# Kernel tuning notes

Measured on AMD Instinct MI355X. Metric: run time of the kernel, lower is better.

Reference implementation:

```python
import jax, jax.numpy as jnp
import numpy as np
from jax import lax

M, B, D = 32, 64, 8192  # history length, batch of systems, degrees of freedom


def setup_inputs() -> dict:
    key = jax.random.key(0)
    k1, k2, k3 = jax.random.split(key, 3)
    s = jax.random.normal(k1, (M, B, D), dtype=jnp.float32)
    y = jax.random.normal(k2, (M, B, D), dtype=jnp.float32)
    frc = jax.random.normal(k3, (B, D), dtype=jnp.float32)
    return {"s": s, "y": y, "frc": frc}


def reference(s, y, frc):
    # r_i = 1 / (s_i . y_i), per batch row, as stored by extend()
    r = 1.0 / jnp.sum(s * y, axis=-1, keepdims=True)  # [M, B, 1]

    # First loop: iterate history from newest (i = M-1) to oldest (i = 0)
    def back_step(q, carry):
        si, yi, ri = carry
        ai = ri * jnp.sum(si * q, axis=-1, keepdims=True)  # [B, 1]
        q = q - ai * yi
        return q, ai

    q0 = -frc
    q, a_rev = lax.scan(back_step, q0, (s[::-1], y[::-1], r[::-1]))
    a = a_rev[::-1]  # a[i] now aligned with history index i

    # Initial Hessian scaling gamma = (s_last . y_last) / (y_last . y_last)
    g = (jnp.sum(s[-1] * y[-1], axis=-1) / jnp.sum(y[-1] * y[-1], axis=-1))[:, None]
    q = g * q

    # Second loop: oldest to newest
    def fwd_step(q, carry):
        si, yi, ri, ai = carry
        bi = ri * jnp.sum(yi * q, axis=-1, keepdims=True)
        q = q + si * (ai - bi)
        return q, None

    q, _ = lax.scan(fwd_step, q, (s, y, r, a))
    return -q
```

## Files before the change

### kernel.cpp

```cpp
#include <hip/hip_runtime.h>

#define Mh 32
#define Bh 64
#define Dh 8192
#define KCH 1024
#define NCH (Dh / KCH)

#define OFF_WSY 0
#define OFF_WYY (64 * 1024)
#define OFF_VS  (2 * 64 * 1024)
#define OFF_VY  (OFF_VS + 64 * 32)
#define OFF_CY  (OFF_VY + 64 * 32)
#define OFF_CS  (OFF_CY + 64 * 32)
#define OFF_G   (OFF_CS + 64 * 32)
#define WS_ZERO_FLOATS OFF_CY

__global__ __launch_bounds__(256) void gram_kernel(
    const float* __restrict__ s, const float* __restrict__ y,
    const float* __restrict__ frc, float* __restrict__ ws)
{
    __shared__ float sT[32 * 64];
    __shared__ float yT[32 * 64];
    __shared__ float fT[64];

    const int b  = blockIdx.x & 63;
    const int ch = blockIdx.x >> 6;
    const int k0 = ch * KCH;
    const int t  = threadIdx.x;
    const int w  = t >> 6;
    const int l  = t & 63;
    const int tx = l & 7;
    const int ty = l >> 3;

    float asy[4][4] = {};
    float ayy[4][4] = {};
    float avs[4] = {}, avy[4] = {};

    const int i0 = t >> 4,          k4_0 = t & 15;
    const int i1 = (t + 256) >> 4,  k4_1 = (t + 256) & 15;

    for (int st = 0; st < KCH / 64; ++st) {
        const int kb = k0 + st * 64;
        const float4 sv0 = *(const float4*)(s + ((size_t)i0 * Bh + b) * Dh + kb + (k4_0 << 2));
        const float4 yv0 = *(const float4*)(y + ((size_t)i0 * Bh + b) * Dh + kb + (k4_0 << 2));
        const float4 sv1 = *(const float4*)(s + ((size_t)i1 * Bh + b) * Dh + kb + (k4_1 << 2));
        const float4 yv1 = *(const float4*)(y + ((size_t)i1 * Bh + b) * Dh + kb + (k4_1 << 2));
        float4 fv4 = make_float4(0.f, 0.f, 0.f, 0.f);
        if (t < 16) fv4 = *(const float4*)(frc + (size_t)b * Dh + kb + (t << 2));

        __syncthreads();
        {
            const int kk0 = (k4_0 << 2) ^ (((i0 >> 2) & 7) << 2);
            *(float4*)&sT[i0 * 64 + kk0] = sv0;
            *(float4*)&yT[i0 * 64 + kk0] = yv0;
            const int kk1 = (k4_1 << 2) ^ (((i1 >> 2) & 7) << 2);
            *(float4*)&sT[i1 * 64 + kk1] = sv1;
            *(float4*)&yT[i1 * 64 + kk1] = yv1;
            if (t < 16) *(float4*)&fT[t << 2] = fv4;
        }
        __syncthreads();

        #pragma unroll
        for (int kk = 0; kk < 16; kk += 4) {
            const int kc = (w << 4) + kk;
            float4 sv[4], ytv[4], yxv[4];
            #pragma unroll
            for (int aa = 0; aa < 4; ++aa) {
                sv[aa]  = *(const float4*)&sT[((ty << 2) + aa) * 64 + (kc ^ (ty << 2))];
                ytv[aa] = *(const float4*)&yT[((ty << 2) + aa) * 64 + (kc ^ (ty << 2))];
                yxv[aa] = *(const float4*)&yT[((tx << 2) + aa) * 64 + (kc ^ (tx << 2))];
            }
            const float4 fv = *(const float4*)&fT[kc];
            #pragma unroll
            for (int aa = 0; aa < 4; ++aa) {
                #pragma unroll
                for (int cc = 0; cc < 4; ++cc) {
                    asy[aa][cc] += sv[aa].x * yxv[cc].x + sv[aa].y * yxv[cc].y
                                 + sv[aa].z * yxv[cc].z + sv[aa].w * yxv[cc].w;
                    ayy[aa][cc] += ytv[aa].x * yxv[cc].x + ytv[aa].y * yxv[cc].y
                                 + ytv[aa].z * yxv[cc].z + ytv[aa].w * yxv[cc].w;
                }
                avs[aa] += sv[aa].x * fv.x + sv[aa].y * fv.y + sv[aa].z * fv.z + sv[aa].w * fv.w;
                avy[aa] += ytv[aa].x * fv.x + ytv[aa].y * fv.y + ytv[aa].z * fv.z + ytv[aa].w * fv.w;
            }
        }
    }

    __syncthreads();
    for (int wv = 0; wv < 4; ++wv) {
        if (w == wv) {
            #pragma unroll
            for (int aa = 0; aa < 4; ++aa) {
                #pragma unroll
                for (int cc = 0; cc < 4; ++cc) {
                    const int e = ((ty << 2) + aa) * 32 + (tx << 2) + cc;
                    if (wv == 0) { sT[e] = asy[aa][cc];  yT[e] = ayy[aa][cc]; }
                    else         { sT[e] += asy[aa][cc]; yT[e] += ayy[aa][cc]; }
                }
                if (tx == 0) {
                    const int i = (ty << 2) + aa;
                    if (wv == 0) { fT[i] = avs[aa];  fT[32 + i] = avy[aa]; }
                    else         { fT[i] += avs[aa]; fT[32 + i] += avy[aa]; }
                }
            }
        }
        __syncthreads();
    }

    float* WSY = ws + OFF_WSY + b * 1024;
    float* WYY = ws + OFF_WYY + b * 1024;
    for (int e = t; e < 1024; e += 256) {
        unsafeAtomicAdd(&WSY[e], sT[e]);
        unsafeAtomicAdd(&WYY[e], yT[e]);
    }
    if (t < 32)      unsafeAtomicAdd(&ws[OFF_VS + b * 32 + t], fT[t]);
    else if (t < 64) unsafeAtomicAdd(&ws[OFF_VY + b * 32 + (t - 32)], fT[t]);
}

__global__ __launch_bounds__(64) void recur_kernel(float* __restrict__ ws)
{
    const int b    = blockIdx.x;
    const int lane = threadIdx.x;
    const int i    = lane & 31;

    const float* WSY = ws + OFF_WSY + b * 1024;
    const float* WYY = ws + OFF_WYY + b * 1024;

    float row_sy[32], col_sy[32], row_yy[32];
    #pragma unroll
    for (int j = 0; j < 32; ++j) {
        row_sy[j] = WSY[i * 32 + j];
        col_sy[j] = WSY[j * 32 + i];
        row_yy[j] = WYY[i * 32 + j];
    }

    const double r = 1.0 / (double)row_sy[i];
    double acc = -(double)ws[OFF_VS + b * 32 + i];
    double a_val = 0.0;
    #pragma unroll
    for (int j = 31; j >= 0; --j) {
        const double aj = __shfl(r, j) * __shfl(acc, j);
        if (i == j) a_val = aj;
        if (i < j)  acc -= aj * (double)row_sy[j];
    }

    const double g = (double)WSY[31 * 32 + 31] / (double)WYY[31 * 32 + 31];

    double u = -(double)ws[OFF_VY + b * 32 + i];
    #pragma unroll
    for (int j = 0; j < 32; ++j)
        u -= __shfl(a_val, j) * (double)row_yy[j];
    u *= g;

    double tt = u;
    double b_val = 0.0;
    #pragma unroll
    for (int j = 0; j < 32; ++j) {
        const double bj = __shfl(r, j) * __shfl(tt, j);
        if (i == j) b_val = bj;
        const double dj = __shfl(a_val, j) - bj;
        if (i > j) tt += dj * (double)col_sy[j];
    }

    if (lane < 32) {
        ws[OFF_CY + b * 32 + i] = (float)(g * a_val);
        ws[OFF_CS + b * 32 + i] = (float)(b_val - a_val);
    }
    if (lane == 0) ws[OFF_G + b] = (float)g;
}

__global__ __launch_bounds__(256) void combine_kernel(
    const float* __restrict__ s, const float* __restrict__ y,
    const float* __restrict__ frc, const float* __restrict__ ws,
    float* __restrict__ out)
{
    __shared__ float cy[32], cs[32];
    const int b  = blockIdx.x & 63;
    const int ch = blockIdx.x >> 6;
    const int t  = threadIdx.x;
    if (t < 32) { cy[t] = ws[OFF_CY + b * 32 + t]; cs[t] = ws[OFF_CS + b * 32 + t]; }
    __syncthreads();

    const int d = ch * 1024 + (t << 2);
    const float g = ws[OFF_G + b];
    const float4 fv = *(const float4*)(frc + (size_t)b * Dh + d);
    float4 acc;
    acc.x = g * fv.x; acc.y = g * fv.y; acc.z = g * fv.z; acc.w = g * fv.w;

    #pragma unroll 8
    for (int i = 0; i < 32; ++i) {
        const float4 yv = *(const float4*)(y + ((size_t)i * Bh + b) * Dh + d);
        const float4 sv = *(const float4*)(s + ((size_t)i * Bh + b) * Dh + d);
        const float a1 = cy[i], a2 = cs[i];
        acc.x += a1 * yv.x + a2 * sv.x;
        acc.y += a1 * yv.y + a2 * sv.y;
        acc.z += a1 * yv.z + a2 * sv.z;
        acc.w += a1 * yv.w + a2 * sv.w;
    }
    *(float4*)(out + (size_t)b * Dh + d) = acc;
}

extern "C" void kernel_launch(void* const* d_in, const int* in_sizes, int n_in,
                              void* d_out, int out_size, void* d_ws, size_t ws_size,
                              hipStream_t stream)
{
    const float* s   = (const float*)d_in[0];
    const float* y   = (const float*)d_in[1];
    const float* frc = (const float*)d_in[2];
    float* out = (float*)d_out;
    float* ws  = (float*)d_ws;

    hipMemsetAsync(d_ws, 0, (size_t)WS_ZERO_FLOATS * sizeof(float), stream);

    gram_kernel<<<dim3(Bh * NCH), dim3(256), 0, stream>>>(s, y, frc, ws);
    recur_kernel<<<dim3(Bh), dim3(64), 0, stream>>>(ws);
    combine_kernel<<<dim3(Bh * NCH), dim3(256), 0, stream>>>(s, y, frc, ws, out);
}
```

Measured before the change: 232.7 us.

## Prefetch gram tiles, replace atomics with partial buffers, batch combine loads

The gram kernel now stages 128-wide tiles and issues the global loads for the next stage into registers while computing the current one. Per-chunk partial Gram matrices are written to separate workspace slots instead of being atomically accumulated. This removes the memset and the atomics, and the recurrence kernel now reduces the eight partials in shared memory. The combine kernel groups 8 history loads at a time to raise memory-level parallelism. The trade-offs are more registers, more LDS, and an extra workspace read in the recurrence kernel.

```diff
diff --git a/kernel.cpp b/kernel.cpp
--- a/kernel.cpp
+++ b/kernel.cpp
@@ -5,23 +5,24 @@
 #define Dh 8192
 #define KCH 1024
 #define NCH (Dh / KCH)
-
-#define OFF_WSY 0
-#define OFF_WYY (64 * 1024)
-#define OFF_VS  (2 * 64 * 1024)
-#define OFF_VY  (OFF_VS + 64 * 32)
-#define OFF_CY  (OFF_VY + 64 * 32)
-#define OFF_CS  (OFF_CY + 64 * 32)
-#define OFF_G   (OFF_CS + 64 * 32)
-#define WS_ZERO_FLOATS OFF_CY
+#define STG 128
+#define NST (KCH / STG)
+
+#define OFF_PSY 0
+#define OFF_PYY 524288
+#define OFF_PVS 1048576
+#define OFF_PVY (OFF_PVS + 16384)
+#define OFF_CY  (OFF_PVY + 16384)
+#define OFF_CS  (OFF_CY + 2048)
+#define OFF_G   (OFF_CS + 2048)
 
 __global__ __launch_bounds__(256) void gram_kernel(
     const float* __restrict__ s, const float* __restrict__ y,
     const float* __restrict__ frc, float* __restrict__ ws)
 {
-    __shared__ float sT[32 * 64];
-    __shared__ float yT[32 * 64];
-    __shared__ float fT[64];
+    __shared__ float sT[32 * STG];
+    __shared__ float yT[32 * STG];
+    __shared__ float fT[STG];
 
     const int b  = blockIdx.x & 63;
     const int ch = blockIdx.x >> 6;
@@ -31,57 +32,66 @@
     const int l  = t & 63;
     const int tx = l & 7;
     const int ty = l >> 3;
+    const size_t base = (size_t)b * Dh;
 
     float asy[4][4] = {};
     float ayy[4][4] = {};
     float avs[4] = {}, avy[4] = {};
 
-    const int i0 = t >> 4,          k4_0 = t & 15;
-    const int i1 = (t + 256) >> 4,  k4_1 = (t + 256) & 15;
-
-    for (int st = 0; st < KCH / 64; ++st) {
-        const int kb = k0 + st * 64;
-        const float4 sv0 = *(const float4*)(s + ((size_t)i0 * Bh + b) * Dh + kb + (k4_0 << 2));
-        const float4 yv0 = *(const float4*)(y + ((size_t)i0 * Bh + b) * Dh + kb + (k4_0 << 2));
-        const float4 sv1 = *(const float4*)(s + ((size_t)i1 * Bh + b) * Dh + kb + (k4_1 << 2));
-        const float4 yv1 = *(const float4*)(y + ((size_t)i1 * Bh + b) * Dh + kb + (k4_1 << 2));
-        float4 fv4 = make_float4(0.f, 0.f, 0.f, 0.f);
-        if (t < 16) fv4 = *(const float4*)(frc + (size_t)b * Dh + kb + (t << 2));
-
+    int ri[4], rc[4];
+    #pragma unroll
+    for (int rep = 0; rep < 4; ++rep) {
+        const int idx = t + rep * 256;
+        ri[rep] = idx >> 5;
+        rc[rep] = idx & 31;
+    }
+
+    float4 pS[4], pY[4], pF;
+    auto issue = [&](int kb) {
+        #pragma unroll
+        for (int rep = 0; rep < 4; ++rep) {
+            const size_t off = ((size_t)ri[rep] * Bh) * Dh + base + kb + (rc[rep] << 2);
+            pS[rep] = *(const float4*)(s + off);
+            pY[rep] = *(const float4*)(y + off);
+        }
+        if (t < 32) pF = *(const float4*)(frc + base + kb + (t << 2));
+    };
+
+    issue(k0);
+    for (int st = 0; st < NST; ++st) {
         __syncthreads();
-        {
-            const int kk0 = (k4_0 << 2) ^ (((i0 >> 2) & 7) << 2);
-            *(float4*)&sT[i0 * 64 + kk0] = sv0;
-            *(float4*)&yT[i0 * 64 + kk0] = yv0;
-            const int kk1 = (k4_1 << 2) ^ (((i1 >> 2) & 7) << 2);
-            *(float4*)&sT[i1 * 64 + kk1] = sv1;
-            *(float4*)&yT[i1 * 64 + kk1] = yv1;
-            if (t < 16) *(float4*)&fT[t << 2] = fv4;
-        }
+        #pragma unroll
+        for (int rep = 0; rep < 4; ++rep) {
+            const int col = rc[rep] ^ ((ri[rep] >> 2) & 7);
+            *(float4*)&sT[ri[rep] * STG + (col << 2)] = pS[rep];
+            *(float4*)&yT[ri[rep] * STG + (col << 2)] = pY[rep];
+        }
+        if (t < 32) *(float4*)&fT[t << 2] = pF;
         __syncthreads();
-
-        #pragma unroll
-        for (int kk = 0; kk < 16; kk += 4) {
-            const int kc = (w << 4) + kk;
-            float4 sv[4], ytv[4], yxv[4];
+        if (st + 1 < NST) issue(k0 + (st + 1) * STG);
+
+        #pragma unroll
+        for (int kk = 0; kk < 8; ++kk) {
+            const int c0 = (w << 3) + kk;
+            float4 sv[4], tv[4], xv[4];
             #pragma unroll
             for (int aa = 0; aa < 4; ++aa) {
-                sv[aa]  = *(const float4*)&sT[((ty << 2) + aa) * 64 + (kc ^ (ty << 2))];
-                ytv[aa] = *(const float4*)&yT[((ty << 2) + aa) * 64 + (kc ^ (ty << 2))];
-                yxv[aa] = *(const float4*)&yT[((tx << 2) + aa) * 64 + (kc ^ (tx << 2))];
+                sv[aa] = *(const float4*)&sT[((ty << 2) + aa) * STG + ((c0 ^ ty) << 2)];
+                tv[aa] = *(const float4*)&yT[((ty << 2) + aa) * STG + ((c0 ^ ty) << 2)];
+                xv[aa] = *(const float4*)&yT[((tx << 2) + aa) * STG + ((c0 ^ tx) << 2)];
             }
-            const float4 fv = *(const float4*)&fT[kc];
+            const float4 fv = *(const float4*)&fT[c0 << 2];
             #pragma unroll
             for (int aa = 0; aa < 4; ++aa) {
                 #pragma unroll
                 for (int cc = 0; cc < 4; ++cc) {
-                    asy[aa][cc] += sv[aa].x * yxv[cc].x + sv[aa].y * yxv[cc].y
-                                 + sv[aa].z * yxv[cc].z + sv[aa].w * yxv[cc].w;
-                    ayy[aa][cc] += ytv[aa].x * yxv[cc].x + ytv[aa].y * yxv[cc].y
-                                 + ytv[aa].z * yxv[cc].z + ytv[aa].w * yxv[cc].w;
+                    asy[aa][cc] += sv[aa].x * xv[cc].x + sv[aa].y * xv[cc].y
+                                 + sv[aa].z * xv[cc].z + sv[aa].w * xv[cc].w;
+                    ayy[aa][cc] += tv[aa].x * xv[cc].x + tv[aa].y * xv[cc].y
+                                 + tv[aa].z * xv[cc].z + tv[aa].w * xv[cc].w;
                 }
                 avs[aa] += sv[aa].x * fv.x + sv[aa].y * fv.y + sv[aa].z * fv.z + sv[aa].w * fv.w;
-                avy[aa] += ytv[aa].x * fv.x + ytv[aa].y * fv.y + ytv[aa].z * fv.z + ytv[aa].w * fv.w;
+                avy[aa] += tv[aa].x * fv.x + tv[aa].y * fv.y + tv[aa].z * fv.z + tv[aa].w * fv.w;
             }
         }
     }
@@ -107,25 +117,44 @@
         __syncthreads();
     }
 
-    float* WSY = ws + OFF_WSY + b * 1024;
-    float* WYY = ws + OFF_WYY + b * 1024;
-    for (int e = t; e < 1024; e += 256) {
-        unsafeAtomicAdd(&WSY[e], sT[e]);
-        unsafeAtomicAdd(&WYY[e], yT[e]);
-    }
-    if (t < 32)      unsafeAtomicAdd(&ws[OFF_VS + b * 32 + t], fT[t]);
-    else if (t < 64) unsafeAtomicAdd(&ws[OFF_VY + b * 32 + (t - 32)], fT[t]);
-}
-
-__global__ __launch_bounds__(64) void recur_kernel(float* __restrict__ ws)
-{
-    const int b    = blockIdx.x;
-    const int lane = threadIdx.x;
-    const int i    = lane & 31;
-
-    const float* WSY = ws + OFF_WSY + b * 1024;
-    const float* WYY = ws + OFF_WYY + b * 1024;
-
+    float* PSY = ws + OFF_PSY + ((size_t)ch * Bh + b) * 1024;
+    float* PYY = ws + OFF_PYY + ((size_t)ch * Bh + b) * 1024;
+    *(float4*)&PSY[t << 2] = *(const float4*)&sT[t << 2];
+    *(float4*)&PYY[t << 2] = *(const float4*)&yT[t << 2];
+    if (t < 32)      ws[OFF_PVS + (ch * 64 + b) * 32 + t] = fT[t];
+    else if (t < 64) ws[OFF_PVY + (ch * 64 + b) * 32 + (t - 32)] = fT[t];
+}
+
+__global__ __launch_bounds__(256) void recur_kernel(float* __restrict__ ws)
+{
+    __shared__ float WSY[1024], WYY[1024], VS[32], VY[32];
+    const int b = blockIdx.x;
+    const int t = threadIdx.x;
+
+    float4 a4 = make_float4(0.f, 0.f, 0.f, 0.f);
+    float4 c4 = make_float4(0.f, 0.f, 0.f, 0.f);
+    #pragma unroll
+    for (int ch = 0; ch < NCH; ++ch) {
+        const float4 u = *(const float4*)&ws[OFF_PSY + ((size_t)ch * Bh + b) * 1024 + (t << 2)];
+        const float4 v = *(const float4*)&ws[OFF_PYY + ((size_t)ch * Bh + b) * 1024 + (t << 2)];
+        a4.x += u.x; a4.y += u.y; a4.z += u.z; a4.w += u.w;
+        c4.x += v.x; c4.y += v.y; c4.z += v.z; c4.w += v.w;
+    }
+    *(float4*)&WSY[t << 2] = a4;
+    *(float4*)&WYY[t << 2] = c4;
+    if (t < 32) {
+        float av = 0.f, cv = 0.f;
+        #pragma unroll
+        for (int ch = 0; ch < NCH; ++ch) {
+            av += ws[OFF_PVS + (ch * 64 + b) * 32 + t];
+            cv += ws[OFF_PVY + (ch * 64 + b) * 32 + t];
+        }
+        VS[t] = av; VY[t] = cv;
+    }
+    __syncthreads();
+    if (t >= 64) return;
+
+    const int i = t & 31;
     float row_sy[32], col_sy[32], row_yy[32];
     #pragma unroll
     for (int j = 0; j < 32; ++j) {
@@ -135,7 +164,7 @@
     }
 
     const double r = 1.0 / (double)row_sy[i];
-    double acc = -(double)ws[OFF_VS + b * 32 + i];
+    double acc = -(double)VS[i];
     double a_val = 0.0;
     #pragma unroll
     for (int j = 31; j >= 0; --j) {
@@ -146,7 +175,7 @@
 
     const double g = (double)WSY[31 * 32 + 31] / (double)WYY[31 * 32 + 31];
 
-    double u = -(double)ws[OFF_VY + b * 32 + i];
+    double u = -(double)VY[i];
     #pragma unroll
     for (int j = 0; j < 32; ++j)
         u -= __shfl(a_val, j) * (double)row_yy[j];
@@ -162,11 +191,11 @@
         if (i > j) tt += dj * (double)col_sy[j];
     }
 
-    if (lane < 32) {
+    if (t < 32) {
         ws[OFF_CY + b * 32 + i] = (float)(g * a_val);
         ws[OFF_CS + b * 32 + i] = (float)(b_val - a_val);
     }
-    if (lane == 0) ws[OFF_G + b] = (float)g;
+    if (t == 0) ws[OFF_G + b] = (float)g;
 }
 
 __global__ __launch_bounds__(256) void combine_kernel(
@@ -182,22 +211,33 @@
     __syncthreads();
 
     const int d = ch * 1024 + (t << 2);
+    const size_t base = (size_t)b * Dh + d;
     const float g = ws[OFF_G + b];
-    const float4 fv = *(const float4*)(frc + (size_t)b * Dh + d);
+    const float4 fv = *(const float4*)(frc + base);
     float4 acc;
     acc.x = g * fv.x; acc.y = g * fv.y; acc.z = g * fv.z; acc.w = g * fv.w;
 
-    #pragma unroll 8
-    for (int i = 0; i < 32; ++i) {
-        const float4 yv = *(const float4*)(y + ((size_t)i * Bh + b) * Dh + d);
-        const float4 sv = *(const float4*)(s + ((size_t)i * Bh + b) * Dh + d);
-        const float a1 = cy[i], a2 = cs[i];
-        acc.x += a1 * yv.x + a2 * sv.x;
-        acc.y += a1 * yv.y + a2 * sv.y;
-        acc.z += a1 * yv.z + a2 * sv.z;
-        acc.w += a1 * yv.w + a2 * sv.w;
-    }
-    *(float4*)(out + (size_t)b * Dh + d) = acc;
+    const float* py = y + base;
+    const float* ps = s + base;
+    #pragma unroll
+    for (int grp = 0; grp < 4; ++grp) {
+        float4 yv[8], sv[8];
+        #pragma unroll
+        for (int j = 0; j < 8; ++j) {
+            const size_t off = (size_t)(grp * 8 + j) * ((size_t)Bh * Dh);
+            yv[j] = *(const float4*)(py + off);
+            sv[j] = *(const float4*)(ps + off);
+        }
+        #pragma unroll
+        for (int j = 0; j < 8; ++j) {
+            const float a1 = cy[grp * 8 + j], a2 = cs[grp * 8 + j];
+            acc.x += a1 * yv[j].x + a2 * sv[j].x;
+            acc.y += a1 * yv[j].y + a2 * sv[j].y;
+            acc.z += a1 * yv[j].z + a2 * sv[j].z;
+            acc.w += a1 * yv[j].w + a2 * sv[j].w;
+        }
+    }
+    *(float4*)(out + base) = acc;
 }
 
 extern "C" void kernel_launch(void* const* d_in, const int* in_sizes, int n_in,
@@ -210,9 +250,7 @@
     float* out = (float*)d_out;
     float* ws  = (float*)d_ws;
 
-    hipMemsetAsync(d_ws, 0, (size_t)WS_ZERO_FLOATS * sizeof(float), stream);
-
     gram_kernel<<<dim3(Bh * NCH), dim3(256), 0, stream>>>(s, y, frc, ws);
-    recur_kernel<<<dim3(Bh), dim3(64), 0, stream>>>(ws);
+    recur_kernel<<<dim3(Bh), dim3(256), 0, stream>>>(ws);
     combine_kernel<<<dim3(Bh * NCH), dim3(256), 0, stream>>>(s, y, frc, ws, out);
 }
```

After: 255.7 us. +9.9%, slower.
